# Kernel tuning notes

Measured on AMD Instinct MI355X. Metric: run time of the kernel, lower is better.

The kernel has to match this reference:

```python
import jax, jax.numpy as jnp
import numpy as np

H, O, E, V = 128, 128, 512, 34
B, T, L = 64, 2048, 256


def _lstm(x, wih, whh, bih, bhh):
    # x: [T, B, Din] -> outputs [T, B, H]; PyTorch gate order i, f, g, o
    n = whh.shape[1]
    h0 = jnp.zeros((x.shape[1], n), x.dtype)
    b = bih + bhh
    def step(carry, xt):
        h, c = carry
        g = xt @ wih.T + h @ whh.T + b
        i, f, gg, o = jnp.split(g, 4, axis=-1)
        c = jax.nn.sigmoid(f) * c + jax.nn.sigmoid(i) * jnp.tanh(gg)
        h = jax.nn.sigmoid(o) * jnp.tanh(c)
        return (h, c), h
    _, ys = jax.lax.scan(step, (h0, h0), x)
    return ys


def _conv1d_s2(x, w, b):
    # x: [B, Cin, T], w: [Cout, Cin, 2], kernel=2 stride=2 valid
    y = jax.lax.conv_general_dilated(x, w, (2,), 'VALID', dimension_numbers=('NCH', 'OIH', 'NCH'))
    return y + b[None, :, None]


def setup_inputs():
    key = jax.random.key(0)
    ctr = [0]
    def mk(shape, s=0.05):
        ctr[0] += 1
        return jax.random.normal(jax.random.fold_in(key, ctr[0]), shape, dtype=jnp.float32) * s
    inp = {}
    inp['utter'] = mk((B, T, 40), 1.0)
    inp['targets'] = jax.random.randint(jax.random.fold_in(key, 999), (B, L), 0, V)
    inp['wih_f'] = mk((4 * H, 40)); inp['whh_f'] = mk((4 * H, H)); inp['bih_f'] = mk((4 * H,)); inp['bhh_f'] = mk((4 * H,))
    inp['wih_r'] = mk((4 * H, 40)); inp['whh_r'] = mk((4 * H, H)); inp['bih_r'] = mk((4 * H,)); inp['bhh_r'] = mk((4 * H,))
    inp['c1w'] = mk((H, 2 * H, 2)); inp['c1b'] = mk((H,))
    inp['wih1'] = mk((4 * H, H)); inp['whh1'] = mk((4 * H, H)); inp['bih1'] = mk((4 * H,)); inp['bhh1'] = mk((4 * H,))
    inp['c2w'] = mk((H, H, 2)); inp['c2b'] = mk((H,))
    inp['wih2'] = mk((4 * H, H)); inp['whh2'] = mk((4 * H, H)); inp['bih2'] = mk((4 * H,)); inp['bhh2'] = mk((4 * H,))
    inp['kw'] = mk((O, H)); inp['kb'] = mk((O,)); inp['vw'] = mk((O, H)); inp['vb'] = mk((O,))
    inp['wihd'] = mk((4 * O, O + E)); inp['whhd'] = mk((4 * O, O)); inp['bihd'] = mk((4 * O,)); inp['bhhd'] = mk((4 * O,))
    inp['w1'] = mk((V, O)); inp['b1'] = mk((V,)); inp['w2'] = mk((V, O)); inp['b2'] = mk((V,))
    inp['w3'] = mk((V, V)); inp['b3'] = mk((V,))
    inp['emb'] = mk((V, E), 1.0)
    inp['sh0'] = mk((B, O)); inp['sc0'] = mk((B, O))
    return inp


def _forward(utter, targets, wih_f, whh_f, bih_f, bhh_f, wih_r, whh_r, bih_r, bhh_r,
             c1w, c1b, wih1, whh1, bih1, bhh1, c2w, c2b, wih2, whh2, bih2, bhh2,
             kw, kb, vw, vb, wihd, whhd, bihd, bhhd, w1, b1, w2, b2, w3, b3,
             emb, sh0, sc0):
    # ---- Listener (encoder) ----
    x = jnp.transpose(utter, (1, 0, 2))            # [T, B, 40]
    fwd = _lstm(x, wih_f, whh_f, bih_f, bhh_f)
    bwd = _lstm(x[::-1], wih_r, whh_r, bih_r, bhh_r)[::-1]
    h = jnp.concatenate([fwd, bwd], axis=-1)       # [T, B, 2H]
    h = jnp.transpose(h, (1, 2, 0))                # [B, 2H, T]
    h = _conv1d_s2(h, c1w, c1b)                    # [B, H, T/2]
    h = jnp.transpose(h, (2, 0, 1))                # [T/2, B, H]
    h = _lstm(h, wih1, whh1, bih1, bhh1)
    h = jnp.transpose(h, (1, 2, 0))
    h = _conv1d_s2(h, c2w, c2b)                    # [B, H, T/4]
    h = jnp.transpose(h, (2, 0, 1))
    h = _lstm(h, wih2, whh2, bih2, bhh2)
    h = jnp.transpose(h, (1, 0, 2))                # [B, T/4, H]
    hk = h @ kw.T + kb                              # [B, T/4, O]
    hv = h @ vw.T + vb
    # ---- Speller (decoder) ----
    ys = jnp.transpose(emb[targets], (1, 0, 2))[:-1]   # [L-1, B, E]
    mask = jnp.ones((utter.shape[0], hk.shape[1]), utter.dtype)  # all full-length
    bd = bihd + bhhd
    def step(carry, y_in):
        c, sh, sc = carry
        g = jnp.concatenate([y_in, c], axis=1) @ wihd.T + sh @ whhd.T + bd
        i, f, gg, o = jnp.split(g, 4, axis=-1)
        sc_n = jax.nn.sigmoid(f) * sc + jax.nn.sigmoid(i) * jnp.tanh(gg)
        sh_n = jax.nn.sigmoid(o) * jnp.tanh(sc_n)
        # NOTE: original attends with the cell state sc (faithful to source)
        att = jax.nn.softmax(jnp.einsum('btd,bd->bt', hk, sc_n), axis=1) * mask
        att = att / jnp.sum(att, axis=1, keepdims=True)
        c_n = jnp.einsum('bt,btd->bd', att, hv)
        out = jax.nn.relu(sh_n @ w1.T + b1 + c_n @ w2.T + b2)
        out = jax.nn.softmax(out @ w3.T + b3, axis=1)
        return (c_n, sh_n, sc_n), out
    c0 = jnp.zeros_like(sh0)
    _, preds = jax.lax.scan(step, (c0, sh0, sc0), ys)
    return jnp.transpose(preds, (1, 0, 2))         # [B, L-1, V]


def reference(utter, targets, wih_f, whh_f, bih_f, bhh_f, wih_r, whh_r, bih_r, bhh_r,
              c1w, c1b, wih1, whh1, bih1, bhh1, c2w, c2b, wih2, whh2, bih2, bhh2,
              kw, kb, vw, vb, wihd, whhd, bihd, bhhd, w1, b1, w2, b2, w3, b3,
              emb, sh0, sc0):
    return _forward(utter, targets, wih_f, whh_f, bih_f, bhh_f, wih_r, whh_r, bih_r, bhh_r,
                    c1w, c1b, wih1, whh1, bih1, bhh1, c2w, c2b, wih2, whh2, bih2, bhh2,
                    kw, kb, vw, vb, wihd, whhd, bihd, bhhd, w1, b1, w2, b2, w3, b3,
                    emb, sh0, sc0)
```

## Files before the change

### kernel.cpp

```cpp
#include <hip/hip_runtime.h>

typedef _Float16 half_t;
typedef _Float16 __attribute__((ext_vector_type(2))) half2_t;

__device__ __forceinline__ float fdot2_(half2_t a, half2_t b, float c) {
#if __has_builtin(__builtin_amdgcn_fdot2)
    return __builtin_amdgcn_fdot2(a, b, c, false);
#else
    return c + (float)a[0] * (float)b[0] + (float)a[1] * (float)b[1];
#endif
}
__device__ __forceinline__ half2_t h2(float a, float b) {
    half2_t r; r[0] = (half_t)a; r[1] = (half_t)b; return r;
}
__device__ __forceinline__ half2_t bc2(unsigned int u) {
    return __builtin_bit_cast(half2_t, u);
}
__device__ __forceinline__ float sigm(float x) { return 1.0f / (1.0f + __expf(-x)); }
__device__ __forceinline__ float tanh_(float x) { return 1.0f - 2.0f / (1.0f + __expf(2.0f * x)); }
__device__ __forceinline__ unsigned int packbf2(float a, float b) {
    unsigned int ua = __float_as_uint(a);
    ua = (ua + 0x7fffu + ((ua >> 16) & 1u)) >> 16;
    unsigned int ub = __float_as_uint(b);
    ub = (ub + 0x7fffu + ((ub >> 16) & 1u)) >> 16;
    return ua | (ub << 16);
}
__device__ __forceinline__ float blo(unsigned int u) { return __uint_as_float(u << 16); }
__device__ __forceinline__ float bhi(unsigned int u) { return __uint_as_float(u & 0xffff0000u); }

__global__ __launch_bounds__(512) void lstm1_k(
    const float* __restrict__ utter,
    const float* __restrict__ wih_f, const float* __restrict__ whh_f,
    const float* __restrict__ bih_f, const float* __restrict__ bhh_f,
    const float* __restrict__ wih_r, const float* __restrict__ whh_r,
    const float* __restrict__ bih_r, const float* __restrict__ bhh_r,
    float* __restrict__ Hf, float* __restrict__ Hr)
{
    const int tid = threadIdx.x;
    const int b   = blockIdx.x & 63;
    const int dir = blockIdx.x >> 6;
    const float* wih = dir ? wih_r : wih_f;
    const float* whh = dir ? whh_r : whh_f;
    const float* bih = dir ? bih_r : bih_f;
    const float* bhh = dir ? bhh_r : bhh_f;
    float* Hout = dir ? Hr : Hf;

    __shared__ float gates[512];
    __shared__ __align__(16) half_t h_h[128];
    __shared__ __align__(16) half_t x2[3][48];

    const int j = tid;
    half2_t wr2[64];
    {
        const float4* wp = reinterpret_cast<const float4*>(whh + j * 128);
#pragma unroll
        for (int m = 0; m < 32; ++m) {
            float4 v = wp[m];
            wr2[2 * m]     = h2(v.x, v.y);
            wr2[2 * m + 1] = h2(v.z, v.w);
        }
    }
    half2_t wx2[20];
    {
        const float4* xp = reinterpret_cast<const float4*>(wih + j * 40);
#pragma unroll
        for (int q = 0; q < 10; ++q) {
            float4 v = xp[q];
            wx2[2 * q]     = h2(v.x, v.y);
            wx2[2 * q + 1] = h2(v.z, v.w);
        }
    }
    const float bias = bih[j] + bhh[j];
    float c = 0.0f;
    if (tid < 128) h_h[tid] = (half_t)0.0f;
    if (tid < 40) {
        int tt0 = dir ? 2047 : 0;
        x2[0][tid] = (half_t)utter[((size_t)b * 2048 + tt0) * 40 + tid];
    } else if (tid < 80) {
        int tt1 = dir ? 2046 : 1;
        x2[1][tid - 40] = (half_t)utter[((size_t)b * 2048 + tt1) * 40 + (tid - 40)];
    }
    __syncthreads();

    for (int t = 0; t < 2048; ++t) {
        const int cur = t % 3;
        const int nx2 = (t + 2) % 3;
        float xn = 0.0f;
        const int tq = tid - 128;
        if (tq >= 0 && tq < 40) {
            int tn = (t + 2 < 2048) ? (t + 2) : 2047;
            int ttn = dir ? (2047 - tn) : tn;
            xn = utter[((size_t)b * 2048 + ttn) * 40 + tq];
        }
        float g0 = bias, g1 = 0.f, g2 = 0.f, g3 = 0.f;
        {
            const uint4* x4p = reinterpret_cast<const uint4*>(&x2[cur][0]);
#pragma unroll
            for (int q = 0; q < 5; ++q) {
                uint4 u = x4p[q];
                g0 = fdot2_(wx2[4 * q],     bc2(u.x), g0);
                g1 = fdot2_(wx2[4 * q + 1], bc2(u.y), g1);
                g2 = fdot2_(wx2[4 * q + 2], bc2(u.z), g2);
                g3 = fdot2_(wx2[4 * q + 3], bc2(u.w), g3);
            }
            const uint4* h4p = reinterpret_cast<const uint4*>(h_h);
#pragma unroll
            for (int q = 0; q < 16; ++q) {
                uint4 u = h4p[q];
                g0 = fdot2_(wr2[4 * q],     bc2(u.x), g0);
                g1 = fdot2_(wr2[4 * q + 1], bc2(u.y), g1);
                g2 = fdot2_(wr2[4 * q + 2], bc2(u.z), g2);
                g3 = fdot2_(wr2[4 * q + 3], bc2(u.w), g3);
            }
        }
        gates[j] = (g0 + g1) + (g2 + g3);
        __syncthreads();
        if (tid < 128) {
            float i_ = sigm(gates[tid]);
            float f_ = sigm(gates[128 + tid]);
            float g_ = tanh_(gates[256 + tid]);
            float o_ = sigm(gates[384 + tid]);
            c = f_ * c + i_ * g_;
            float hh = o_ * tanh_(c);
            h_h[tid] = (half_t)hh;
            int tt = dir ? (2047 - t) : t;
            Hout[((size_t)tt * 64 + b) * 128 + tid] = hh;
        } else if (tq < 40) {
            x2[nx2][tq] = (half_t)xn;
        }
        __syncthreads();
    }
}

__global__ __launch_bounds__(512) void lstm_k(
    const float* __restrict__ P, const float* __restrict__ whh,
    float* __restrict__ Hout, int T)
{
    const int tid = threadIdx.x;
    const int b = blockIdx.x;
    const int j = tid;
    __shared__ float gates[512];
    __shared__ __align__(16) half_t h_h[128];
    half2_t wr2[64];
    {
        const float4* wp = reinterpret_cast<const float4*>(whh + j * 128);
#pragma unroll
        for (int m = 0; m < 32; ++m) {
            float4 v = wp[m];
            wr2[2 * m]     = h2(v.x, v.y);
            wr2[2 * m + 1] = h2(v.z, v.w);
        }
    }
    float c = 0.0f;
    if (tid < 128) h_h[tid] = (half_t)0.0f;
    float p_cur = P[((size_t)b * T + 0) * 512 + j];
    float p_n1  = P[((size_t)b * T + ((T > 1) ? 1 : 0)) * 512 + j];
    __syncthreads();
    for (int t = 0; t < T; ++t) {
        int tn = (t + 2 < T) ? (t + 2) : (T - 1);
        float p_n2 = P[((size_t)b * T + tn) * 512 + j];
        float g0 = p_cur, g1 = 0.f, g2 = 0.f, g3 = 0.f;
        const uint4* h4p = reinterpret_cast<const uint4*>(h_h);
#pragma unroll
        for (int q = 0; q < 16; ++q) {
            uint4 u = h4p[q];
            g0 = fdot2_(wr2[4 * q],     bc2(u.x), g0);
            g1 = fdot2_(wr2[4 * q + 1], bc2(u.y), g1);
            g2 = fdot2_(wr2[4 * q + 2], bc2(u.z), g2);
            g3 = fdot2_(wr2[4 * q + 3], bc2(u.w), g3);
        }
        gates[j] = (g0 + g1) + (g2 + g3);
        __syncthreads();
        if (tid < 128) {
            float i_ = sigm(gates[tid]);
            float f_ = sigm(gates[128 + tid]);
            float g_ = tanh_(gates[256 + tid]);
            float o_ = sigm(gates[384 + tid]);
            c = f_ * c + i_ * g_;
            float hh = o_ * tanh_(c);
            h_h[tid] = (half_t)hh;
            Hout[((size_t)t * 64 + b) * 128 + tid] = hh;
        }
        __syncthreads();
        p_cur = p_n1;
        p_n1 = p_n2;
    }
}

template <int CIN>
__global__ __launch_bounds__(128) void conv_k(
    const float* __restrict__ HA, const float* __restrict__ HB,
    const float* __restrict__ W, const float* __restrict__ bias,
    float* __restrict__ out, int Tout)
{
    __shared__ __align__(16) float xin[64 * CIN];
    const int b = blockIdx.x;
    const int t0 = blockIdx.y * 32;
    const int tid = threadIdx.x;
    for (int idx = tid; idx < 64 * CIN; idx += 128) {
        int tl = idx / CIN, ci = idx % CIN;
        int tau = t0 * 2 + tl;
        float v;
        if constexpr (CIN == 256) {
            v = (ci < 128) ? HA[(size_t)tau * 8192 + b * 128 + ci]
                           : HB[(size_t)tau * 8192 + b * 128 + (ci - 128)];
        } else {
            v = HA[(size_t)tau * 8192 + b * 128 + ci];
        }
        xin[idx] = v;
    }
    __syncthreads();
    const int co = tid;
    float acc[32];
#pragma unroll
    for (int u = 0; u < 32; ++u) acc[u] = 0.0f;
    const float4* Wrow4 = reinterpret_cast<const float4*>(W + (size_t)co * 2 * CIN);
    const float4* xin4 = reinterpret_cast<const float4*>(xin);
    for (int c4 = 0; c4 < CIN / 4; ++c4) {
        float4 wA = Wrow4[2 * c4];
        float4 wB = Wrow4[2 * c4 + 1];
#pragma unroll
        for (int u = 0; u < 32; ++u) {
            float4 x0 = xin4[(2 * u) * (CIN / 4) + c4];
            float4 x1 = xin4[(2 * u + 1) * (CIN / 4) + c4];
            acc[u] += wA.x * x0.x + wA.y * x1.x + wA.z * x0.y + wA.w * x1.y
                    + wB.x * x0.z + wB.y * x1.z + wB.z * x0.w + wB.w * x1.w;
        }
    }
    float bs = bias[co];
#pragma unroll
    for (int u = 0; u < 32; ++u)
        out[((size_t)b * Tout + t0 + u) * 128 + co] = acc[u] + bs;
}

__global__ __launch_bounds__(256) void gemm_k(
    const float* __restrict__ A, const float* __restrict__ W, int ldw,
    const float* __restrict__ bias1, const float* __restrict__ bias2,
    float* __restrict__ C, int M, int N, int K, int mode, int Tdim)
{
    __shared__ __align__(16) float As[16][68];
    __shared__ __align__(16) float Ws[16][68];
    const int tid = threadIdx.x;
    const int m0 = blockIdx.x * 64, n0 = blockIdx.y * 64;
    const int kk = tid & 15, mm = tid >> 4;
    const int tm = tid & 15, tn = tid >> 4;
    float acc[4][4];
#pragma unroll
    for (int i = 0; i < 4; ++i)
#pragma unroll
        for (int jj = 0; jj < 4; ++jj) acc[i][jj] = 0.0f;

    for (int k0 = 0; k0 < K; k0 += 16) {
#pragma unroll
        for (int r = 0; r < 4; ++r) {
            As[kk][mm + 16 * r] = A[(size_t)(m0 + mm + 16 * r) * K + k0 + kk];
            Ws[kk][mm + 16 * r] = W[(size_t)(n0 + mm + 16 * r) * ldw + k0 + kk];
        }
        __syncthreads();
#pragma unroll
        for (int q = 0; q < 16; ++q) {
            float4 a = reinterpret_cast<const float4*>(&As[q][0])[tm];
            float4 w = reinterpret_cast<const float4*>(&Ws[q][0])[tn];
            acc[0][0] += a.x * w.x; acc[0][1] += a.x * w.y; acc[0][2] += a.x * w.z; acc[0][3] += a.x * w.w;
            acc[1][0] += a.y * w.x; acc[1][1] += a.y * w.y; acc[1][2] += a.y * w.z; acc[1][3] += a.y * w.w;
            acc[2][0] += a.z * w.x; acc[2][1] += a.z * w.y; acc[2][2] += a.z * w.z; acc[2][3] += a.z * w.w;
            acc[3][0] += a.w * w.x; acc[3][1] += a.w * w.y; acc[3][2] += a.w * w.z; acc[3][3] += a.w * w.w;
        }
        __syncthreads();
    }
    float bv[4];
#pragma unroll
    for (int jj = 0; jj < 4; ++jj) {
        int n = n0 + tn * 4 + jj;
        float v = 0.0f;
        if (bias1) v += bias1[n];
        if (bias2) v += bias2[n];
        bv[jj] = v;
    }
#pragma unroll
    for (int i = 0; i < 4; ++i) {
        int m = m0 + tm * 4 + i;
#pragma unroll
        for (int jj = 0; jj < 4; ++jj) {
            int n = n0 + tn * 4 + jj;
            float v = acc[i][jj] + bv[jj];
            if (mode == 0) {
                C[(size_t)m * N + n] = v;
            } else {
                int bb = m & 63, tt = m >> 6;
                C[((size_t)bb * N + n) * Tdim + tt] = v;
            }
        }
    }
}

__global__ __launch_bounds__(512) void packemb_k(
    const int* __restrict__ targets, const float* __restrict__ emb,
    float* __restrict__ Ypack)
{
    int m = blockIdx.x;
    int l = m >> 6, b = m & 63;
    int tgt = targets[b * 256 + l];
    Ypack[(size_t)m * 512 + threadIdx.x] = emb[(size_t)tgt * 512 + threadIdx.x];
}

__global__ __launch_bounds__(1024) void decoder_k(
    const float* __restrict__ Yp, const float* __restrict__ whhd, const float* __restrict__ wihd,
    const float* __restrict__ hk,
    const float* __restrict__ hv,
    const float* __restrict__ w1, const float* __restrict__ b1,
    const float* __restrict__ w2, const float* __restrict__ b2,
    const float* __restrict__ w3, const float* __restrict__ b3,
    const float* __restrict__ sh0, const float* __restrict__ sc0,
    float* __restrict__ out)
{
    __shared__ unsigned int hk_lds[512][66];
    __shared__ __align__(16) float partial[32][128];
    __shared__ __align__(16) float sh_f[128];
    __shared__ __align__(16) half_t sh_h[128];
    __shared__ __align__(16) float sc_f[128];
    __shared__ __align__(16) float c_f[128];
    __shared__ __align__(16) half_t c_h[128];
    __shared__ __align__(16) float att[512];
    __shared__ float red[8];
    __shared__ float pa[34], pb[34], z_lds[34];
    __shared__ float w3_lds[34 * 34];
    __shared__ float b3_lds[34];

    const int tid = threadIdx.x;
    const int b = blockIdx.x;
    const int role = tid >> 9;
    const int j = tid & 511;
    float* pflat = &partial[0][0];

    half2_t w2r[64];
    {
        const float4* wp = role
            ? reinterpret_cast<const float4*>(wihd + (size_t)j * 640 + 512)
            : reinterpret_cast<const float4*>(whhd + (size_t)j * 128);
#pragma unroll
        for (int m = 0; m < 32; ++m) {
            float4 v = wp[m];
            w2r[2 * m]     = h2(v.x, v.y);
            w2r[2 * m + 1] = h2(v.z, v.w);
        }
    }
    {
        const float4* hp = reinterpret_cast<const float4*>(hk + ((size_t)j * 64 + b) * 128 + role * 64);
#pragma unroll
        for (int q = 0; q < 16; ++q) {
            float4 v = hp[q];
            hk_lds[j][role * 32 + 2 * q]     = packbf2(v.x, v.y);
            hk_lds[j][role * 32 + 2 * q + 1] = packbf2(v.z, v.w);
        }
    }
    for (int idx = tid; idx < 34 * 34; idx += 1024) w3_lds[idx] = w3[idx];
    if (tid < 34) b3_lds[tid] = b3[tid];
    float sc_r = 0.0f;
    if (tid < 128) {
        float s = sh0[b * 128 + tid];
        sh_f[tid] = s; sh_h[tid] = (half_t)s;
        sc_r = sc0[b * 128 + tid];
        sc_f[tid] = sc_r;
        c_f[tid] = 0.0f; c_h[tid] = (half_t)0.0f;
    }
    __syncthreads();

    const int wid = tid >> 6, lane = tid & 63;
    const int tg = tid >> 5, dq = tid & 31;
    float yp_cur = (role == 0) ? Yp[(size_t)b * 512 + j] : 0.0f;

    for (int l = 0; l < 255; ++l) {
        int lnxt = (l + 1 < 255) ? (l + 1) : l;
        float yp_nxt = (role == 0) ? Yp[((size_t)lnxt * 64 + b) * 512 + j] : 0.0f;
        {
            const uint4* s4 = reinterpret_cast<const uint4*>(role ? c_h : sh_h);
            float g0 = yp_cur, g1 = 0.f, g2 = 0.f, g3 = 0.f;
#pragma unroll
            for (int q = 0; q < 16; ++q) {
                uint4 u = s4[q];
                g0 = fdot2_(w2r[4 * q],     bc2(u.x), g0);
                g1 = fdot2_(w2r[4 * q + 1], bc2(u.y), g1);
                g2 = fdot2_(w2r[4 * q + 2], bc2(u.z), g2);
                g3 = fdot2_(w2r[4 * q + 3], bc2(u.w), g3);
            }
            pflat[tid] = (g0 + g1) + (g2 + g3);
        }
        __syncthreads();
        if (tid < 128) {
            float i_ = sigm(pflat[tid]       + pflat[512 + tid]);
            float f_ = sigm(pflat[128 + tid] + pflat[640 + tid]);
            float g_ = tanh_(pflat[256 + tid] + pflat[768 + tid]);
            float o_ = sigm(pflat[384 + tid] + pflat[896 + tid]);
            sc_r = f_ * sc_r + i_ * g_;
            float hh = o_ * tanh_(sc_r);
            sh_f[tid] = hh; sh_h[tid] = (half_t)hh;
            sc_f[tid] = sc_r;
        }
        __syncthreads();
        if (tid < 512) {
            float e0 = 0.f, e1 = 0.f, e2 = 0.f, e3 = 0.f;
            const uint2* hkr = reinterpret_cast<const uint2*>(&hk_lds[tid][0]);
            const float4* sc4 = reinterpret_cast<const float4*>(sc_f);
#pragma unroll
            for (int q = 0; q < 32; ++q) {
                uint2 u = hkr[q];
                float4 s = sc4[q];
                e0 += blo(u.x) * s.x; e1 += bhi(u.x) * s.y;
                e2 += blo(u.y) * s.z; e3 += bhi(u.y) * s.w;
            }
            float p = __expf((e0 + e1) + (e2 + e3));
            att[tid] = p;
            float ps = p;
#pragma unroll
            for (int off = 32; off; off >>= 1) ps += __shfl_xor(ps, off);
            if (lane == 0) red[wid] = ps;
        }
        __syncthreads();
        {
            const float* hvp = hv + ((size_t)(tg * 16) * 64 + b) * 128 + dq * 4;
            float4 a = make_float4(0.f, 0.f, 0.f, 0.f);
#pragma unroll 4
            for (int tt = 0; tt < 16; ++tt) {
                float w = att[tg * 16 + tt];
                float4 v = *reinterpret_cast<const float4*>(hvp + (size_t)tt * 8192);
                a.x += w * v.x; a.y += w * v.y; a.z += w * v.z; a.w += w * v.w;
            }
            *reinterpret_cast<float4*>(&partial[tg][dq * 4]) = a;
        }
        __syncthreads();
        if (tid < 128) {
            float S = ((red[0] + red[1]) + (red[2] + red[3]))
                    + ((red[4] + red[5]) + (red[6] + red[7]));
            float cs = 0.f;
#pragma unroll
            for (int g = 0; g < 32; ++g) cs += partial[g][tid];
            float cv = cs / S;
            c_f[tid] = cv; c_h[tid] = (half_t)cv;
        }
        __syncthreads();
        if (tid < 34) {
            float o1 = b1[tid];
            const float4* w1r = reinterpret_cast<const float4*>(w1 + tid * 128);
            const float4* sh4 = reinterpret_cast<const float4*>(sh_f);
#pragma unroll 8
            for (int q = 0; q < 32; ++q) {
                float4 a = w1r[q], h = sh4[q];
                o1 += a.x * h.x + a.y * h.y + a.z * h.z + a.w * h.w;
            }
            pa[tid] = o1;
        } else if (tid >= 64 && tid < 98) {
            int v = tid - 64;
            float o2 = b2[v];
            const float4* w2p = reinterpret_cast<const float4*>(w2 + v * 128);
            const float4* c4 = reinterpret_cast<const float4*>(c_f);
#pragma unroll 8
            for (int q = 0; q < 32; ++q) {
                float4 a = w2p[q], cc = c4[q];
                o2 += a.x * cc.x + a.y * cc.y + a.z * cc.z + a.w * cc.w;
            }
            pb[v] = o2;
        }
        __syncthreads();
        if (tid < 34) {
            float z = b3_lds[tid];
            const float* w3r = &w3_lds[tid * 34];
            for (int v = 0; v < 34; ++v) z += w3r[v] * fmaxf(pa[v] + pb[v], 0.0f);
            z_lds[tid] = z;
        }
        __syncthreads();
        if (tid < 34) {
            float zm = z_lds[0];
            for (int v = 1; v < 34; ++v) zm = fmaxf(zm, z_lds[v]);
            float Ssum = 0.0f;
            for (int v = 0; v < 34; ++v) Ssum += __expf(z_lds[v] - zm);
            out[((size_t)b * 255 + l) * 34 + tid] = __expf(z_lds[tid] - zm) / Ssum;
        }
        yp_cur = yp_nxt;
        __syncthreads();
    }
}

extern "C" void kernel_launch(void* const* d_in, const int* in_sizes, int n_in,
                              void* d_out, int out_size, void* d_ws, size_t ws_size,
                              hipStream_t stream) {
    (void)in_sizes; (void)n_in; (void)out_size; (void)ws_size;
    const float* utter = (const float*)d_in[0];
    const int*   targets = (const int*)d_in[1];
    const float* wih_f = (const float*)d_in[2];
    const float* whh_f = (const float*)d_in[3];
    const float* bih_f = (const float*)d_in[4];
    const float* bhh_f = (const float*)d_in[5];
    const float* wih_r = (const float*)d_in[6];
    const float* whh_r = (const float*)d_in[7];
    const float* bih_r = (const float*)d_in[8];
    const float* bhh_r = (const float*)d_in[9];
    const float* c1w = (const float*)d_in[10];
    const float* c1b = (const float*)d_in[11];
    const float* wih1 = (const float*)d_in[12];
    const float* whh1 = (const float*)d_in[13];
    const float* bih1 = (const float*)d_in[14];
    const float* bhh1 = (const float*)d_in[15];
    const float* c2w = (const float*)d_in[16];
    const float* c2b = (const float*)d_in[17];
    const float* wih2 = (const float*)d_in[18];
    const float* whh2 = (const float*)d_in[19];
    const float* bih2 = (const float*)d_in[20];
    const float* bhh2 = (const float*)d_in[21];
    const float* kw = (const float*)d_in[22];
    const float* kb = (const float*)d_in[23];
    const float* vw = (const float*)d_in[24];
    const float* vb = (const float*)d_in[25];
    const float* wihd = (const float*)d_in[26];
    const float* whhd = (const float*)d_in[27];
    const float* bihd = (const float*)d_in[28];
    const float* bhhd = (const float*)d_in[29];
    const float* w1 = (const float*)d_in[30];
    const float* b1 = (const float*)d_in[31];
    const float* w2 = (const float*)d_in[32];
    const float* b2 = (const float*)d_in[33];
    const float* w3 = (const float*)d_in[34];
    const float* b3 = (const float*)d_in[35];
    const float* emb = (const float*)d_in[36];
    const float* sh0 = (const float*)d_in[37];
    const float* sc0 = (const float*)d_in[38];

    char* ws = (char*)d_ws;
    const size_t MB = 1ull << 20;
    float* Hf       = (float*)(ws + 0);
    float* Hr       = (float*)(ws + 64 * MB);
    float* conv1out = (float*)(ws + 128 * MB);
    float* P2       = (float*)(ws + 0);
    float* H2       = (float*)(ws + 128 * MB);
    float* conv2out = (float*)(ws + 0);
    float* P3       = (float*)(ws + 16 * MB);
    float* H3       = (float*)(ws + 80 * MB);
    float* hkb      = (float*)(ws + 96 * MB);
    float* hvb      = (float*)(ws + 112 * MB);
    float* Ypack    = (float*)(ws + 128 * MB);
    float* Yp       = (float*)(ws + 16 * MB);

    lstm1_k<<<128, 512, 0, stream>>>(utter, wih_f, whh_f, bih_f, bhh_f,
                                     wih_r, whh_r, bih_r, bhh_r, Hf, Hr);
    conv_k<256><<<dim3(64, 32), 128, 0, stream>>>(Hf, Hr, c1w, c1b, conv1out, 1024);
    gemm_k<<<dim3(1024, 8), 256, 0, stream>>>(conv1out, wih1, 128, bih1, bhh1,
                                              P2, 65536, 512, 128, 0, 0);
    lstm_k<<<64, 512, 0, stream>>>(P2, whh1, H2, 1024);
    conv_k<128><<<dim3(64, 16), 128, 0, stream>>>(H2, nullptr, c2w, c2b, conv2out, 512);
    gemm_k<<<dim3(512, 8), 256, 0, stream>>>(conv2out, wih2, 128, bih2, bhh2,
                                             P3, 32768, 512, 128, 0, 0);
    lstm_k<<<64, 512, 0, stream>>>(P3, whh2, H3, 512);
    gemm_k<<<dim3(512, 2), 256, 0, stream>>>(H3, kw, 128, kb, nullptr,
                                             hkb, 32768, 128, 128, 0, 0);
    gemm_k<<<dim3(512, 2), 256, 0, stream>>>(H3, vw, 128, vb, nullptr,
                                             hvb, 32768, 128, 128, 0, 0);
    packemb_k<<<16320, 512, 0, stream>>>(targets, emb, Ypack);
    gemm_k<<<dim3(255, 8), 256, 0, stream>>>(Ypack, wihd, 640, bihd, bhhd,
                                             Yp, 16320, 512, 512, 0, 0);
    decoder_k<<<64, 1024, 0, stream>>>(Yp, whhd, wihd, hkb, hvb,
                                       w1, b1, w2, b2, w3, b3, sh0, sc0,
                                       (float*)d_out);
}
```

Before: 5.999 ms.

## Split LSTM recurrent dot products across 1024 threads with prepacked fp16 weights

Recurrent weights are prepacked to fp16 pairs in a workspace by new pack kernels and streamed from global/cache each step instead of held in registers. Each LSTM block goes to 1024 threads, with two threads splitting each gate's hidden-state dot product and summing partials in LDS. Intermediate hidden states and input projections are stored as fp16 to cut memory traffic, the decoder's value matrix is transposed and packed to bf16 for a different attention-context reduction, and one barrier is dropped from the decoder loop. This trades register pressure for per-step global/L1 weight reloads and adds precision loss from fp16/bf16 intermediates.

Result: slower. 7.498 ms (+25.0%).

```diff
diff --git a/kernel.cpp b/kernel.cpp
--- a/kernel.cpp
+++ b/kernel.cpp
@@ -15,6 +15,9 @@
 }
 __device__ __forceinline__ half2_t bc2(unsigned int u) {
     return __builtin_bit_cast(half2_t, u);
+}
+__device__ __forceinline__ unsigned int pk2(float a, float b) {
+    return __builtin_bit_cast(unsigned int, h2(a, b));
 }
 __device__ __forceinline__ float sigm(float x) { return 1.0f / (1.0f + __expf(-x)); }
 __device__ __forceinline__ float tanh_(float x) { return 1.0f - 2.0f / (1.0f + __expf(2.0f * x)); }
@@ -28,49 +31,45 @@
 __device__ __forceinline__ float blo(unsigned int u) { return __uint_as_float(u << 16); }
 __device__ __forceinline__ float bhi(unsigned int u) { return __uint_as_float(u & 0xffff0000u); }
 
-__global__ __launch_bounds__(512) void lstm1_k(
+#define ATTRS1024 __attribute__((amdgpu_flat_work_group_size(1024, 1024))) \
+                  __attribute__((amdgpu_waves_per_eu(4, 4)))
+
+__global__ __launch_bounds__(256) void packrow_k(
+    const float* __restrict__ src, unsigned int* __restrict__ dst,
+    int srcCols, int colOff, int pairs, int total)
+{
+    int idx = blockIdx.x * 256 + threadIdx.x;
+    if (idx >= total) return;
+    int j = idx / pairs, q = idx % pairs;
+    const float* s = src + (size_t)j * srcCols + colOff + 2 * q;
+    dst[idx] = pk2(s[0], s[1]);
+}
+
+__global__ ATTRS1024 void lstm1_k(
     const float* __restrict__ utter,
-    const float* __restrict__ wih_f, const float* __restrict__ whh_f,
+    const unsigned int* __restrict__ Wl1,
+    const unsigned int* __restrict__ Wx,
     const float* __restrict__ bih_f, const float* __restrict__ bhh_f,
-    const float* __restrict__ wih_r, const float* __restrict__ whh_r,
     const float* __restrict__ bih_r, const float* __restrict__ bhh_r,
-    float* __restrict__ Hf, float* __restrict__ Hr)
+    unsigned short* __restrict__ Hf, unsigned short* __restrict__ Hr)
 {
     const int tid = threadIdx.x;
     const int b   = blockIdx.x & 63;
     const int dir = blockIdx.x >> 6;
-    const float* wih = dir ? wih_r : wih_f;
-    const float* whh = dir ? whh_r : whh_f;
+    const int role = tid >> 9;
+    const int j = tid & 511;
+    unsigned short* Hout = dir ? Hr : Hf;
     const float* bih = dir ? bih_r : bih_f;
     const float* bhh = dir ? bhh_r : bhh_f;
-    float* Hout = dir ? Hr : Hf;
-
-    __shared__ float gates[512];
+
+    __shared__ float pflat[1024];
     __shared__ __align__(16) half_t h_h[128];
     __shared__ __align__(16) half_t x2[3][48];
 
-    const int j = tid;
-    half2_t wr2[64];
-    {
-        const float4* wp = reinterpret_cast<const float4*>(whh + j * 128);
-#pragma unroll
-        for (int m = 0; m < 32; ++m) {
-            float4 v = wp[m];
-            wr2[2 * m]     = h2(v.x, v.y);
-            wr2[2 * m + 1] = h2(v.z, v.w);
-        }
-    }
-    half2_t wx2[20];
-    {
-        const float4* xp = reinterpret_cast<const float4*>(wih + j * 40);
-#pragma unroll
-        for (int q = 0; q < 10; ++q) {
-            float4 v = xp[q];
-            wx2[2 * q]     = h2(v.x, v.y);
-            wx2[2 * q + 1] = h2(v.z, v.w);
-        }
-    }
-    const float bias = bih[j] + bhh[j];
+    const uint4* wr4 = reinterpret_cast<const uint4*>(Wl1 + ((size_t)((dir * 2 + role) * 512 + j)) * 32);
+    const uint4* wx4 = reinterpret_cast<const uint4*>(Wx + ((size_t)(dir * 512 + j)) * 20);
+    const float bias = (role == 0) ? (bih[j] + bhh[j]) : 0.0f;
+
     float c = 0.0f;
     if (tid < 128) h_h[tid] = (half_t)0.0f;
     if (tid < 40) {
@@ -86,100 +85,109 @@
         const int cur = t % 3;
         const int nx2 = (t + 2) % 3;
         float xn = 0.0f;
-        const int tq = tid - 128;
-        if (tq >= 0 && tq < 40) {
+        const int sidx = tid - 640;
+        if (sidx >= 0 && sidx < 40) {
             int tn = (t + 2 < 2048) ? (t + 2) : 2047;
             int ttn = dir ? (2047 - tn) : tn;
-            xn = utter[((size_t)b * 2048 + ttn) * 40 + tq];
+            xn = utter[((size_t)b * 2048 + ttn) * 40 + sidx];
         }
         float g0 = bias, g1 = 0.f, g2 = 0.f, g3 = 0.f;
+        if (role == 0) {
+            const uint4* x4 = reinterpret_cast<const uint4*>(&x2[cur][0]);
+#pragma unroll
+            for (int q = 0; q < 5; ++q) {
+                uint4 w = wx4[q];
+                uint4 u = x4[q];
+                g0 = fdot2_(bc2(w.x), bc2(u.x), g0);
+                g1 = fdot2_(bc2(w.y), bc2(u.y), g1);
+                g2 = fdot2_(bc2(w.z), bc2(u.z), g2);
+                g3 = fdot2_(bc2(w.w), bc2(u.w), g3);
+            }
+        }
         {
-            const uint4* x4p = reinterpret_cast<const uint4*>(&x2[cur][0]);
-#pragma unroll
-            for (int q = 0; q < 5; ++q) {
-                uint4 u = x4p[q];
-                g0 = fdot2_(wx2[4 * q],     bc2(u.x), g0);
-                g1 = fdot2_(wx2[4 * q + 1], bc2(u.y), g1);
-                g2 = fdot2_(wx2[4 * q + 2], bc2(u.z), g2);
-                g3 = fdot2_(wx2[4 * q + 3], bc2(u.w), g3);
-            }
-            const uint4* h4p = reinterpret_cast<const uint4*>(h_h);
-#pragma unroll
-            for (int q = 0; q < 16; ++q) {
-                uint4 u = h4p[q];
-                g0 = fdot2_(wr2[4 * q],     bc2(u.x), g0);
-                g1 = fdot2_(wr2[4 * q + 1], bc2(u.y), g1);
-                g2 = fdot2_(wr2[4 * q + 2], bc2(u.z), g2);
-                g3 = fdot2_(wr2[4 * q + 3], bc2(u.w), g3);
-            }
-        }
-        gates[j] = (g0 + g1) + (g2 + g3);
+            const uint4* h4 = reinterpret_cast<const uint4*>(h_h) + role * 8;
+#pragma unroll
+            for (int q = 0; q < 8; ++q) {
+                uint4 w = wr4[q];
+                uint4 u = h4[q];
+                g0 = fdot2_(bc2(w.x), bc2(u.x), g0);
+                g1 = fdot2_(bc2(w.y), bc2(u.y), g1);
+                g2 = fdot2_(bc2(w.z), bc2(u.z), g2);
+                g3 = fdot2_(bc2(w.w), bc2(u.w), g3);
+            }
+        }
+        pflat[tid] = (g0 + g1) + (g2 + g3);
         __syncthreads();
         if (tid < 128) {
-            float i_ = sigm(gates[tid]);
-            float f_ = sigm(gates[128 + tid]);
-            float g_ = tanh_(gates[256 + tid]);
-            float o_ = sigm(gates[384 + tid]);
+            float i_ = sigm(pflat[tid]       + pflat[512 + tid]);
+            float f_ = sigm(pflat[128 + tid] + pflat[640 + tid]);
+            float g_ = tanh_(pflat[256 + tid] + pflat[768 + tid]);
+            float o_ = sigm(pflat[384 + tid] + pflat[896 + tid]);
             c = f_ * c + i_ * g_;
             float hh = o_ * tanh_(c);
-            h_h[tid] = (half_t)hh;
+            half_t hx = (half_t)hh;
+            h_h[tid] = hx;
             int tt = dir ? (2047 - t) : t;
-            Hout[((size_t)tt * 64 + b) * 128 + tid] = hh;
-        } else if (tq < 40) {
-            x2[nx2][tq] = (half_t)xn;
-        }
-        __syncthreads();
-    }
-}
-
-__global__ __launch_bounds__(512) void lstm_k(
-    const float* __restrict__ P, const float* __restrict__ whh,
-    float* __restrict__ Hout, int T)
+            Hout[((size_t)tt * 64 + b) * 128 + tid] = __builtin_bit_cast(unsigned short, hx);
+        } else if (sidx >= 0 && sidx < 40) {
+            x2[nx2][sidx] = (half_t)xn;
+        }
+        __syncthreads();
+    }
+}
+
+__global__ ATTRS1024 void lstm_k(
+    const unsigned short* __restrict__ Ph,
+    const unsigned int* __restrict__ Wh,
+    void* __restrict__ Hout, int T, int outHalf)
 {
     const int tid = threadIdx.x;
     const int b = blockIdx.x;
-    const int j = tid;
-    __shared__ float gates[512];
+    const int role = tid >> 9;
+    const int j = tid & 511;
+    __shared__ float pflat[1024];
     __shared__ __align__(16) half_t h_h[128];
-    half2_t wr2[64];
-    {
-        const float4* wp = reinterpret_cast<const float4*>(whh + j * 128);
-#pragma unroll
-        for (int m = 0; m < 32; ++m) {
-            float4 v = wp[m];
-            wr2[2 * m]     = h2(v.x, v.y);
-            wr2[2 * m + 1] = h2(v.z, v.w);
-        }
-    }
+
+    const uint4* wr4 = reinterpret_cast<const uint4*>(Wh + ((size_t)(role * 512 + j)) * 32);
     float c = 0.0f;
     if (tid < 128) h_h[tid] = (half_t)0.0f;
-    float p_cur = P[((size_t)b * T + 0) * 512 + j];
-    float p_n1  = P[((size_t)b * T + ((T > 1) ? 1 : 0)) * 512 + j];
+    float p_cur = 0.f, p_n1 = 0.f;
+    if (role == 0) {
+        p_cur = (float)__builtin_bit_cast(half_t, Ph[((size_t)b * T + 0) * 512 + j]);
+        p_n1  = (float)__builtin_bit_cast(half_t, Ph[((size_t)b * T + ((T > 1) ? 1 : 0)) * 512 + j]);
+    }
     __syncthreads();
     for (int t = 0; t < T; ++t) {
-        int tn = (t + 2 < T) ? (t + 2) : (T - 1);
-        float p_n2 = P[((size_t)b * T + tn) * 512 + j];
+        float p_n2 = 0.f;
+        if (role == 0) {
+            int tn = (t + 2 < T) ? (t + 2) : (T - 1);
+            p_n2 = (float)__builtin_bit_cast(half_t, Ph[((size_t)b * T + tn) * 512 + j]);
+        }
         float g0 = p_cur, g1 = 0.f, g2 = 0.f, g3 = 0.f;
-        const uint4* h4p = reinterpret_cast<const uint4*>(h_h);
-#pragma unroll
-        for (int q = 0; q < 16; ++q) {
-            uint4 u = h4p[q];
-            g0 = fdot2_(wr2[4 * q],     bc2(u.x), g0);
-            g1 = fdot2_(wr2[4 * q + 1], bc2(u.y), g1);
-            g2 = fdot2_(wr2[4 * q + 2], bc2(u.z), g2);
-            g3 = fdot2_(wr2[4 * q + 3], bc2(u.w), g3);
-        }
-        gates[j] = (g0 + g1) + (g2 + g3);
+        const uint4* h4 = reinterpret_cast<const uint4*>(h_h) + role * 8;
+#pragma unroll
+        for (int q = 0; q < 8; ++q) {
+            uint4 w = wr4[q];
+            uint4 u = h4[q];
+            g0 = fdot2_(bc2(w.x), bc2(u.x), g0);
+            g1 = fdot2_(bc2(w.y), bc2(u.y), g1);
+            g2 = fdot2_(bc2(w.z), bc2(u.z), g2);
+            g3 = fdot2_(bc2(w.w), bc2(u.w), g3);
+        }
+        pflat[tid] = (g0 + g1) + (g2 + g3);
         __syncthreads();
         if (tid < 128) {
-            float i_ = sigm(gates[tid]);
-            float f_ = sigm(gates[128 + tid]);
-            float g_ = tanh_(gates[256 + tid]);
-            float o_ = sigm(gates[384 + tid]);
+            float i_ = sigm(pflat[tid]       + pflat[512 + tid]);
+            float f_ = sigm(pflat[128 + tid] + pflat[640 + tid]);
+            float g_ = tanh_(pflat[256 + tid] + pflat[768 + tid]);
+            float o_ = sigm(pflat[384 + tid] + pflat[896 + tid]);
             c = f_ * c + i_ * g_;
             float hh = o_ * tanh_(c);
-            h_h[tid] = (half_t)hh;
-            Hout[((size_t)t * 64 + b) * 128 + tid] = hh;
+            half_t hx = (half_t)hh;
+            h_h[tid] = hx;
+            size_t oi = ((size_t)t * 64 + b) * 128 + tid;
+            if (outHalf) ((unsigned short*)Hout)[oi] = __builtin_bit_cast(unsigned short, hx);
+            else         ((float*)Hout)[oi] = hh;
         }
         __syncthreads();
         p_cur = p_n1;
@@ -189,7 +197,7 @@
 
 template <int CIN>
 __global__ __launch_bounds__(128) void conv_k(
-    const float* __restrict__ HA, const float* __restrict__ HB,
+    const unsigned short* __restrict__ HA, const unsigned short* __restrict__ HB,
     const float* __restrict__ W, const float* __restrict__ bias,
     float* __restrict__ out, int Tout)
 {
@@ -200,14 +208,14 @@
     for (int idx = tid; idx < 64 * CIN; idx += 128) {
         int tl = idx / CIN, ci = idx % CIN;
         int tau = t0 * 2 + tl;
-        float v;
+        unsigned short u;
         if constexpr (CIN == 256) {
-            v = (ci < 128) ? HA[(size_t)tau * 8192 + b * 128 + ci]
+            u = (ci < 128) ? HA[(size_t)tau * 8192 + b * 128 + ci]
                            : HB[(size_t)tau * 8192 + b * 128 + (ci - 128)];
         } else {
-            v = HA[(size_t)tau * 8192 + b * 128 + ci];
-        }
-        xin[idx] = v;
+            u = HA[(size_t)tau * 8192 + b * 128 + ci];
+        }
+        xin[idx] = (float)__builtin_bit_cast(half_t, u);
     }
     __syncthreads();
     const int co = tid;
@@ -236,7 +244,7 @@
 __global__ __launch_bounds__(256) void gemm_k(
     const float* __restrict__ A, const float* __restrict__ W, int ldw,
     const float* __restrict__ bias1, const float* __restrict__ bias2,
-    float* __restrict__ C, int M, int N, int K, int mode, int Tdim)
+    void* __restrict__ C, int M, int N, int K, int mode, int Tdim)
 {
     __shared__ __align__(16) float As[16][68];
     __shared__ __align__(16) float Ws[16][68];
@@ -285,10 +293,13 @@
             int n = n0 + tn * 4 + jj;
             float v = acc[i][jj] + bv[jj];
             if (mode == 0) {
-                C[(size_t)m * N + n] = v;
+                ((float*)C)[(size_t)m * N + n] = v;
+            } else if (mode == 1) {
+                int bb = m & 63, tt = m >> 6;
+                ((float*)C)[((size_t)bb * N + n) * Tdim + tt] = v;
             } else {
-                int bb = m & 63, tt = m >> 6;
-                C[((size_t)bb * N + n) * Tdim + tt] = v;
+                ((unsigned short*)C)[(size_t)m * N + n] =
+                    __builtin_bit_cast(unsigned short, (half_t)v);
             }
         }
     }
@@ -304,10 +315,18 @@
     Ypack[(size_t)m * 512 + threadIdx.x] = emb[(size_t)tgt * 512 + threadIdx.x];
 }
 
-__global__ __launch_bounds__(1024) void decoder_k(
-    const float* __restrict__ Yp, const float* __restrict__ whhd, const float* __restrict__ wihd,
+__global__ __launch_bounds__(256) void packhv_k(
+    const float* __restrict__ hvT, unsigned int* __restrict__ hvpak)
+{
+    int b = blockIdx.x, d = blockIdx.y, i = threadIdx.x;
+    const float2 v = reinterpret_cast<const float2*>(hvT + ((size_t)b * 128 + d) * 512)[i];
+    hvpak[((size_t)b * 128 + d) * 256 + i] = packbf2(v.x, v.y);
+}
+
+__global__ ATTRS1024 void decoder_k(
+    const float* __restrict__ Yp, const unsigned int* __restrict__ Wdec,
     const float* __restrict__ hk,
-    const float* __restrict__ hv,
+    const unsigned int* __restrict__ hvpak,
     const float* __restrict__ w1, const float* __restrict__ b1,
     const float* __restrict__ w2, const float* __restrict__ b2,
     const float* __restrict__ w3, const float* __restrict__ b3,
@@ -315,7 +334,7 @@
     float* __restrict__ out)
 {
     __shared__ unsigned int hk_lds[512][66];
-    __shared__ __align__(16) float partial[32][128];
+    __shared__ float pflat[1024];
     __shared__ __align__(16) float sh_f[128];
     __shared__ __align__(16) half_t sh_h[128];
     __shared__ __align__(16) float sc_f[128];
@@ -331,20 +350,9 @@
     const int b = blockIdx.x;
     const int role = tid >> 9;
     const int j = tid & 511;
-    float* pflat = &partial[0][0];
-
-    half2_t w2r[64];
-    {
-        const float4* wp = role
-            ? reinterpret_cast<const float4*>(wihd + (size_t)j * 640 + 512)
-            : reinterpret_cast<const float4*>(whhd + (size_t)j * 128);
-#pragma unroll
-        for (int m = 0; m < 32; ++m) {
-            float4 v = wp[m];
-            w2r[2 * m]     = h2(v.x, v.y);
-            w2r[2 * m + 1] = h2(v.z, v.w);
-        }
-    }
+
+    const uint4* wd4 = reinterpret_cast<const uint4*>(Wdec + ((size_t)(role * 512 + j)) * 64);
+
     {
         const float4* hp = reinterpret_cast<const float4*>(hk + ((size_t)j * 64 + b) * 128 + role * 64);
 #pragma unroll
@@ -367,22 +375,26 @@
     __syncthreads();
 
     const int wid = tid >> 6, lane = tid & 63;
-    const int tg = tid >> 5, dq = tid & 31;
+    const int g8 = tid >> 7, d = tid & 127;
+    const uint4* hvr = reinterpret_cast<const uint4*>(hvpak + ((size_t)b * 128 + d) * 256 + g8 * 32);
     float yp_cur = (role == 0) ? Yp[(size_t)b * 512 + j] : 0.0f;
 
     for (int l = 0; l < 255; ++l) {
         int lnxt = (l + 1 < 255) ? (l + 1) : l;
         float yp_nxt = (role == 0) ? Yp[((size_t)lnxt * 64 + b) * 512 + j] : 0.0f;
         {
+            float g0 = yp_cur, g1 = 0.f, g2 = 0.f, g3 = 0.f;
             const uint4* s4 = reinterpret_cast<const uint4*>(role ? c_h : sh_h);
-            float g0 = yp_cur, g1 = 0.f, g2 = 0.f, g3 = 0.f;
 #pragma unroll
             for (int q = 0; q < 16; ++q) {
-                uint4 u = s4[q];
-                g0 = fdot2_(w2r[4 * q],     bc2(u.x), g0);
-                g1 = fdot2_(w2r[4 * q + 1], bc2(u.y), g1);
-                g2 = fdot2_(w2r[4 * q + 2], bc2(u.z), g2);
-                g3 = fdot2_(w2r[4 * q + 3], bc2(u.w), g3);
+                uint4 w = wd4[q];
+                uint4 u = s4[q & 3];
+                (void)u;
+                uint4 uu = s4[q];
+                g0 = fdot2_(bc2(w.x), bc2(uu.x), g0);
+                g1 = fdot2_(bc2(w.y), bc2(uu.y), g1);
+                g2 = fdot2_(bc2(w.z), bc2(uu.z), g2);
+                g3 = fdot2_(bc2(w.w), bc2(uu.w), g3);
             }
             pflat[tid] = (g0 + g1) + (g2 + g3);
         }
@@ -418,15 +430,17 @@
         }
         __syncthreads();
         {
-            const float* hvp = hv + ((size_t)(tg * 16) * 64 + b) * 128 + dq * 4;
-            float4 a = make_float4(0.f, 0.f, 0.f, 0.f);
-#pragma unroll 4
-            for (int tt = 0; tt < 16; ++tt) {
-                float w = att[tg * 16 + tt];
-                float4 v = *reinterpret_cast<const float4*>(hvp + (size_t)tt * 8192);
-                a.x += w * v.x; a.y += w * v.y; a.z += w * v.z; a.w += w * v.w;
-            }
-            *reinterpret_cast<float4*>(&partial[tg][dq * 4]) = a;
+            const float4* att4 = reinterpret_cast<const float4*>(att);
+            float acc = 0.0f;
+#pragma unroll
+            for (int q = 0; q < 8; ++q) {
+                uint4 u = hvr[q];
+                float4 a0 = att4[g8 * 16 + 2 * q];
+                float4 a1 = att4[g8 * 16 + 2 * q + 1];
+                acc += blo(u.x) * a0.x + bhi(u.x) * a0.y + blo(u.y) * a0.z + bhi(u.y) * a0.w
+                     + blo(u.z) * a1.x + bhi(u.z) * a1.y + blo(u.w) * a1.z + bhi(u.w) * a1.w;
+            }
+            pflat[tid] = acc;
         }
         __syncthreads();
         if (tid < 128) {
@@ -434,7 +448,7 @@
                     + ((red[4] + red[5]) + (red[6] + red[7]));
             float cs = 0.f;
 #pragma unroll
-            for (int g = 0; g < 32; ++g) cs += partial[g][tid];
+            for (int g = 0; g < 8; ++g) cs += pflat[g * 128 + tid];
             float cv = cs / S;
             c_f[tid] = cv; c_h[tid] = (half_t)cv;
         }
@@ -477,7 +491,6 @@
             out[((size_t)b * 255 + l) * 34 + tid] = __expf(z_lds[tid] - zm) / Ssum;
         }
         yp_cur = yp_nxt;
-        __syncthreads();
     }
 }
 
@@ -527,37 +540,58 @@
 
     char* ws = (char*)d_ws;
     const size_t MB = 1ull << 20;
-    float* Hf       = (float*)(ws + 0);
-    float* Hr       = (float*)(ws + 64 * MB);
-    float* conv1out = (float*)(ws + 128 * MB);
-    float* P2       = (float*)(ws + 0);
-    float* H2       = (float*)(ws + 128 * MB);
-    float* conv2out = (float*)(ws + 0);
-    float* P3       = (float*)(ws + 16 * MB);
-    float* H3       = (float*)(ws + 80 * MB);
-    float* hkb      = (float*)(ws + 96 * MB);
-    float* hvb      = (float*)(ws + 112 * MB);
-    float* Ypack    = (float*)(ws + 128 * MB);
-    float* Yp       = (float*)(ws + 16 * MB);
-
-    lstm1_k<<<128, 512, 0, stream>>>(utter, wih_f, whh_f, bih_f, bhh_f,
-                                     wih_r, whh_r, bih_r, bhh_r, Hf, Hr);
-    conv_k<256><<<dim3(64, 32), 128, 0, stream>>>(Hf, Hr, c1w, c1b, conv1out, 1024);
-    gemm_k<<<dim3(1024, 8), 256, 0, stream>>>(conv1out, wih1, 128, bih1, bhh1,
-                                              P2, 65536, 512, 128, 0, 0);
-    lstm_k<<<64, 512, 0, stream>>>(P2, whh1, H2, 1024);
-    conv_k<128><<<dim3(64, 16), 128, 0, stream>>>(H2, nullptr, c2w, c2b, conv2out, 512);
-    gemm_k<<<dim3(512, 8), 256, 0, stream>>>(conv2out, wih2, 128, bih2, bhh2,
-                                             P3, 32768, 512, 128, 0, 0);
-    lstm_k<<<64, 512, 0, stream>>>(P3, whh2, H3, 512);
+    unsigned int* W = (unsigned int*)(ws + 0);
+    unsigned short* Hf_h   = (unsigned short*)(ws + 1 * MB);
+    unsigned short* Hr_h   = (unsigned short*)(ws + 33 * MB);
+    float*          conv1o = (float*)(ws + 65 * MB);
+    unsigned short* P2_h   = (unsigned short*)(ws + 1 * MB);
+    unsigned short* H2_h   = (unsigned short*)(ws + 65 * MB);
+    float*          conv2o = (float*)(ws + 81 * MB);
+    unsigned short* P3_h   = (unsigned short*)(ws + 97 * MB);
+    float*          H3     = (float*)(ws + 1 * MB);
+    float*          hkb    = (float*)(ws + 17 * MB);
+    float*          hvT    = (float*)(ws + 33 * MB);
+    unsigned int*   hvpak  = (unsigned int*)(ws + 49 * MB);
+    float*          Ypack  = (float*)(ws + 57 * MB);
+    float*          Yp     = (float*)(ws + 89 * MB);
+
+    unsigned int* Wl1 = W + 0;
+    unsigned int* Wx  = W + 65536;
+    unsigned int* Wh2 = W + 86016;
+    unsigned int* Wh3 = W + 118784;
+    unsigned int* Wdec = W + 151552;
+
+    packrow_k<<<64, 256, 0, stream>>>(whh_f, Wl1 + 0,     128, 0,  32, 16384);
+    packrow_k<<<64, 256, 0, stream>>>(whh_f, Wl1 + 16384, 128, 64, 32, 16384);
+    packrow_k<<<64, 256, 0, stream>>>(whh_r, Wl1 + 32768, 128, 0,  32, 16384);
+    packrow_k<<<64, 256, 0, stream>>>(whh_r, Wl1 + 49152, 128, 64, 32, 16384);
+    packrow_k<<<40, 256, 0, stream>>>(wih_f, Wx + 0,      40, 0, 20, 10240);
+    packrow_k<<<40, 256, 0, stream>>>(wih_r, Wx + 10240,  40, 0, 20, 10240);
+    packrow_k<<<64, 256, 0, stream>>>(whh1, Wh2 + 0,     128, 0,  32, 16384);
+    packrow_k<<<64, 256, 0, stream>>>(whh1, Wh2 + 16384, 128, 64, 32, 16384);
+    packrow_k<<<64, 256, 0, stream>>>(whh2, Wh3 + 0,     128, 0,  32, 16384);
+    packrow_k<<<64, 256, 0, stream>>>(whh2, Wh3 + 16384, 128, 64, 32, 16384);
+    packrow_k<<<128, 256, 0, stream>>>(whhd, Wdec + 0,     128, 0,   64, 32768);
+    packrow_k<<<128, 256, 0, stream>>>(wihd, Wdec + 32768, 640, 512, 64, 32768);
+
+    lstm1_k<<<128, 1024, 0, stream>>>(utter, Wl1, Wx, bih_f, bhh_f, bih_r, bhh_r, Hf_h, Hr_h);
+    conv_k<256><<<dim3(64, 32), 128, 0, stream>>>(Hf_h, Hr_h, c1w, c1b, conv1o, 1024);
+    gemm_k<<<dim3(1024, 8), 256, 0, stream>>>(conv1o, wih1, 128, bih1, bhh1,
+                                              P2_h, 65536, 512, 128, 2, 0);
+    lstm_k<<<64, 1024, 0, stream>>>(P2_h, Wh2, H2_h, 1024, 1);
+    conv_k<128><<<dim3(64, 16), 128, 0, stream>>>(H2_h, nullptr, c2w, c2b, conv2o, 512);
+    gemm_k<<<dim3(512, 8), 256, 0, stream>>>(conv2o, wih2, 128, bih2, bhh2,
+                                             P3_h, 32768, 512, 128, 2, 0);
+    lstm_k<<<64, 1024, 0, stream>>>(P3_h, Wh3, H3, 512, 0);
     gemm_k<<<dim3(512, 2), 256, 0, stream>>>(H3, kw, 128, kb, nullptr,
                                              hkb, 32768, 128, 128, 0, 0);
     gemm_k<<<dim3(512, 2), 256, 0, stream>>>(H3, vw, 128, vb, nullptr,
-                                             hvb, 32768, 128, 128, 0, 0);
+                                             hvT, 32768, 128, 128, 1, 512);
+    packhv_k<<<dim3(64, 128), 256, 0, stream>>>(hvT, hvpak);
     packemb_k<<<16320, 512, 0, stream>>>(targets, emb, Ypack);
     gemm_k<<<dim3(255, 8), 256, 0, stream>>>(Ypack, wihd, 640, bihd, bhhd,
                                              Yp, 16320, 512, 512, 0, 0);
-    decoder_k<<<64, 1024, 0, stream>>>(Yp, whhd, wihd, hkb, hvb,
+    decoder_k<<<64, 1024, 0, stream>>>(Yp, Wdec, hkb, hvpak,
                                        w1, b1, w2, b2, w3, b3, sh0, sc0,
                                        (float*)d_out);
 }
```
